# Kernel tuning notes

Measured on AMD Instinct MI355X. Metric: run time of the kernel, lower is better.

Reference implementation:

```python
import jax, jax.numpy as jnp
import numpy as np

DIM = 1024
NUM_HEADS = 16
WINDOW_SIZE = 512
HEAD_DIM = DIM // NUM_HEADS
SCALE = HEAD_DIM ** (-0.5)


def setup_inputs() -> dict:
    key = jax.random.key(0)
    kq, kk, kv = jax.random.split(key, 3)
    shape = (2, NUM_HEADS, 2048, HEAD_DIM)
    q = jax.random.normal(kq, shape, dtype=jnp.float32)
    k = jax.random.normal(kk, shape, dtype=jnp.float32)
    v = jax.random.normal(kv, shape, dtype=jnp.float32)
    return {"q": q, "k": k, "v": v}


def reference(q, k, v):
    B, H, N, D = q.shape
    pos = jnp.arange(N)
    # causal + sliding window: col <= row and col >= row - w + 1
    window_mask = (pos[None, :] <= pos[:, None]) & (pos[None, :] >= pos[:, None] - WINDOW_SIZE + 1)  # (N, N)
    attn = jnp.einsum("bhnd,bhmd->bhnm", q, k) * SCALE  # (B, H, N, N)
    attn = jnp.where(window_mask[None, None], attn, -jnp.inf)
    attn = jax.nn.softmax(attn, axis=-1)
    attn = jnp.nan_to_num(attn, nan=0.0)
    return jnp.einsum("bhnm,bhmd->bhnd", attn, v)
```

## Files before the change

kernel.cpp:

```cpp
#include <hip/hip_runtime.h>
#include <math.h>


#define SEQ 2048
#define HD  64
#define LDR 72

typedef short short8 __attribute__((ext_vector_type(8)));
typedef float f32x4  __attribute__((ext_vector_type(4)));
typedef int   i32x4  __attribute__((ext_vector_type(4)));

static __device__ inline unsigned short f2bf(float f){
  union{float f; unsigned u;} un; un.f=f;
  return (unsigned short)((un.u + 0x7FFFu + ((un.u>>16)&1u))>>16);
}
static __device__ inline int swz(int row){ return (row&3)|(((row>>3)&1)<<2); }

static __device__ __forceinline__ void gll16(const unsigned short* g, unsigned short* l){
  __builtin_amdgcn_global_load_lds(
    (const __attribute__((address_space(1))) unsigned int*)(const void*)g,
    (__attribute__((address_space(3))) unsigned int*)(void*)l, 16, 0, 0);
}

__global__ __launch_bounds__(256) void swa_prep(
    const float* __restrict__ k, const float* __restrict__ v,
    unsigned short* __restrict__ Kb, unsigned short* __restrict__ Vtb)
{
  const int tid=threadIdx.x, bid=blockIdx.x;
  const float C=0.18033688011112042f;

  if(bid<1024){
    const long tbase=(long)bid*4096;
    #pragma unroll
    for(int i=0;i<2;++i){
      int id=i*256+tid, r=id>>3, lc=id&7;
      float4 f0=*(const float4*)(k+tbase+r*64+lc*8);
      float4 f1=*(const float4*)(k+tbase+r*64+lc*8+4);
      unsigned short hh[8];
      hh[0]=f2bf(f0.x*C); hh[1]=f2bf(f0.y*C); hh[2]=f2bf(f0.z*C); hh[3]=f2bf(f0.w*C);
      hh[4]=f2bf(f1.x*C); hh[5]=f2bf(f1.y*C); hh[6]=f2bf(f1.z*C); hh[7]=f2bf(f1.w*C);
      *(uint4*)(Kb+tbase+r*64+(long)((lc^swz(r))*8))=*(uint4*)hh;
    }
  } else {
    __shared__ unsigned short Vs[64*68];
    const long tbase=(long)(bid-1024)*4096;
    #pragma unroll
    for(int i=0;i<2;++i){
      int id=i*256+tid, r=id>>3, c=id&7;
      int phys=(c^(r>>3))&7;
      float4 f0=*(const float4*)(v+tbase+r*64+c*8);
      float4 f1=*(const float4*)(v+tbase+r*64+c*8+4);
      ushort4 a,b;
      a.x=f2bf(f0.x); a.y=f2bf(f0.y); a.z=f2bf(f0.z); a.w=f2bf(f0.w);
      b.x=f2bf(f1.x); b.y=f2bf(f1.y); b.z=f2bf(f1.z); b.w=f2bf(f1.w);
      *(ushort4*)&Vs[r*68+phys*8]  =a;
      *(ushort4*)&Vs[r*68+phys*8+4]=b;
    }
    __syncthreads();
    #pragma unroll
    for(int i=0;i<2;++i){
      int id=i*256+tid, d=id>>3, lc=id&7;
      unsigned short t8[8];
      #pragma unroll
      for(int e=0;e<8;++e){
        int key=lc*8+e;
        int phys=((d>>3)^lc)&7;
        t8[e]=Vs[key*68 + phys*8 + (d&7)];
      }
      *(uint4*)(Vtb+tbase+d*64+(long)((lc^swz(d))*8))=*(uint4*)t8;
    }
  }
}

__global__ __launch_bounds__(512) void swa_main(
    const float* __restrict__ q,
    const unsigned short* __restrict__ Kb,
    const unsigned short* __restrict__ Vtb,
    float* __restrict__ out)
{
  __shared__ unsigned short Ks[2][8192];
  __shared__ unsigned short Vsh[2][8192];

  const int tid=threadIdx.x, bid=blockIdx.x;
  const int mt=bid&7, bh=bid>>3, m0=mt*256;
  const long base=(long)bh*SEQ*HD;
  const int wv=tid>>6, lane=tid&63, quad=lane>>4, l16=lane&15;
  const int qr0=m0+wv*32+l16;

  short8 qa[2][2];
  #pragma unroll
  for(int s=0;s<2;++s){
    const float* qp=q+base+(long)(qr0+s*16)*HD+quad*8;
    #pragma unroll
    for(int kk=0;kk<2;++kk){
      float4 f0=*(const float4*)(qp+kk*32);
      float4 f1=*(const float4*)(qp+kk*32+4);
      short8 a;
      a[0]=(short)f2bf(f0.x); a[1]=(short)f2bf(f0.y);
      a[2]=(short)f2bf(f0.z); a[3]=(short)f2bf(f0.w);
      a[4]=(short)f2bf(f1.x); a[5]=(short)f2bf(f1.y);
      a[6]=(short)f2bf(f1.z); a[7]=(short)f2bf(f1.w);
      qa[s][kk]=a;
    }
  }

  const int rbase=8*(l16>>2)+(l16&3);
  const int swk=(l16&3)|(((l16>>2)&1)<<2);
  const int swv=(l16&3)|(((l16>>3)&1)<<2);
  int kaoff[2][4], vboff[2][4];
  #pragma unroll
  for(int kk=0;kk<2;++kk){
    #pragma unroll
    for(int nt=0;nt<4;++nt)
      kaoff[kk][nt]=(rbase+(nt&1)*4+(nt>>1)*32)*64+(((quad+4*kk)^swk)*8);
    #pragma unroll
    for(int dt=0;dt<4;++dt)
      vboff[kk][dt]=(dt*16+l16)*64+(((quad+4*kk)^swv)*8);
  }

  const unsigned short* Kt=Kb +(long)bh*32*4096;
  const unsigned short* Vt=Vtb+(long)bh*32*4096;
  const int seg=tid*8;

  f32x4 oacc[2][4];
  #pragma unroll
  for(int s=0;s<2;++s)
    #pragma unroll
    for(int dt=0;dt<4;++dt) oacc[s][dt]=(f32x4){0.f,0.f,0.f,0.f};
  float lrun[2]={0.f,0.f};

  const int Tb =4*mt+3;
  const int Tlo=(4*mt>8)?(4*mt-8):0;
  const int npairs=(Tb-Tlo+1)>>1;
  const int myTb =4*mt+(wv>>1);
  const bool clip=(myTb>=8);
  const int myTlo=clip?(myTb-8):0;

  {
    const long o=(long)Tlo*4096;
    gll16(Kt+o+seg,      &Ks[0][seg]);
    gll16(Kt+o+4096+seg, &Ks[0][4096+seg]);
    gll16(Vt+o+seg,      &Vsh[0][seg]);
    gll16(Vt+o+4096+seg, &Vsh[0][4096+seg]);
  }
  __syncthreads();

  for(int p=0;p<npairs;++p){
    const int buf=p&1;
    if(p+1<npairs){
      const long o=(long)(Tlo+2*(p+1))*4096;
      gll16(Kt+o+seg,      &Ks[buf^1][seg]);
      gll16(Kt+o+4096+seg, &Ks[buf^1][4096+seg]);
      gll16(Vt+o+seg,      &Vsh[buf^1][seg]);
      gll16(Vt+o+4096+seg, &Vsh[buf^1][4096+seg]);
    }
    #pragma unroll
    for(int sub=0;sub<2;++sub){
      const int t=Tlo+2*p+sub;
      if(t>=myTlo && t<=myTb){
        const int tb_off=sub*4096;
        short8 ka[2][4], vb[4][2];
        #pragma unroll
        for(int kk=0;kk<2;++kk)
          #pragma unroll
          for(int nt=0;nt<4;++nt)
            ka[kk][nt]=*(const short8*)&Ks[buf][tb_off+kaoff[kk][nt]];
        #pragma unroll
        for(int dt=0;dt<4;++dt)
          #pragma unroll
          for(int kk=0;kk<2;++kk)
            vb[dt][kk]=*(const short8*)&Vsh[buf][tb_off+vboff[kk][dt]];

        const bool msk=(t==myTb)||(clip&&t==myTlo);
        #pragma unroll
        for(int s=0;s<2;++s){
          const int qrow=qr0+s*16;
          f32x4 sacc[4];
          #pragma unroll
          for(int nt=0;nt<4;++nt) sacc[nt]=(f32x4){0.f,0.f,0.f,0.f};
          #pragma unroll
          for(int kk=0;kk<2;++kk)
            #pragma unroll
            for(int nt=0;nt<4;++nt)
              sacc[nt]=__builtin_amdgcn_mfma_f32_16x16x32_bf16(ka[kk][nt],qa[s][kk],sacc[nt],0,0,0);

          unsigned pp[8];
          float ls=0.f;
          #pragma unroll
          for(int nt=0;nt<4;++nt){
            float e0,e1,e2,e3;
            e0=__builtin_amdgcn_exp2f(sacc[nt][0]);
            e1=__builtin_amdgcn_exp2f(sacc[nt][1]);
            e2=__builtin_amdgcn_exp2f(sacc[nt][2]);
            e3=__builtin_amdgcn_exp2f(sacc[nt][3]);
            if(msk){
              const int kb0=t*64+8*quad+(nt&1)*4+(nt>>1)*32;
              #pragma unroll
              for(int r=0;r<4;++r){
                const int key=kb0+r;
                const bool valid=(key<=qrow)&&(key+511>=qrow);
                float* ep=(r==0)?&e0:(r==1)?&e1:(r==2)?&e2:&e3;
                *ep = valid ? *ep : 0.f;
              }
            }
            ls+=e0+e1+e2+e3;
            pp[nt*2+0]=(__float_as_uint(e1)&0xFFFF0000u)|(__float_as_uint(e0)>>16);
            pp[nt*2+1]=(__float_as_uint(e3)&0xFFFF0000u)|(__float_as_uint(e2)>>16);
          }
          lrun[s]+=ls;
          i32x4 i0={(int)pp[0],(int)pp[1],(int)pp[2],(int)pp[3]};
          i32x4 i1={(int)pp[4],(int)pp[5],(int)pp[6],(int)pp[7]};
          short8 pa0=*(short8*)&i0;
          short8 pa1=*(short8*)&i1;
          #pragma unroll
          for(int dt=0;dt<4;++dt){
            oacc[s][dt]=__builtin_amdgcn_mfma_f32_16x16x32_bf16(pa0,vb[dt][0],oacc[s][dt],0,0,0);
            oacc[s][dt]=__builtin_amdgcn_mfma_f32_16x16x32_bf16(pa1,vb[dt][1],oacc[s][dt],0,0,0);
          }
        }
      }
    }
    __syncthreads();
  }

  #pragma unroll
  for(int s=0;s<2;++s){
    float l=lrun[s];
    l+=__shfl_xor(l,16);
    l+=__shfl_xor(l,32);
    float linv=1.0f/l;
    #pragma unroll
    for(int r=0;r<4;++r){
      float lr=__shfl(linv,quad*4+r);
      const int orow=m0+wv*32+s*16+quad*4+r;
      #pragma unroll
      for(int dt=0;dt<4;++dt)
        out[base+(long)orow*HD+dt*16+l16]=oacc[s][dt][r]*lr;
    }
  }
}

__global__ __launch_bounds__(256) void swa_fwd(
    const float* __restrict__ q, const float* __restrict__ k,
    const float* __restrict__ v, float* __restrict__ out)
{
  __shared__ short Qs[64*LDR];
  __shared__ short Ps[64*LDR];
  __shared__ short Ksh[2][64*LDR];
  __shared__ short Vtr[2][HD*LDR];

  const int tid=threadIdx.x, bid=blockIdx.x;
  const int mtile=bid&31, bh=bid>>5, m0=mtile*64;
  const long base=(long)bh*SEQ*HD;
  const int wv=tid>>6, lane=tid&63, quad=lane>>4, l16=lane&15;
  const int dcol=lane;

  {
    const float4* qg=(const float4*)(q+base+(long)m0*HD);
    #pragma unroll
    for(int i=0;i<4;++i){
      int idx=i*256+tid, r=idx>>4, c4=idx&15;
      float4 f=qg[idx];
      ushort4 hh; hh.x=f2bf(f.x); hh.y=f2bf(f.y); hh.z=f2bf(f.z); hh.w=f2bf(f.w);
      *(ushort4*)&Qs[r*LDR+c4*4]=hh;
    }
  }
  const int tb=mtile, tlo=(tb>8)?(tb-8):0;
  float4 kreg[4]; float vcol[4][4];
  {
    const float4* kg=(const float4*)(k+base+(long)(tlo*64)*HD);
    const float*  vg=v+base+(long)(tlo*64)*HD;
    #pragma unroll
    for(int i=0;i<4;++i) kreg[i]=kg[i*256+tid];
    #pragma unroll
    for(int g=0;g<4;++g){ int r0=wv*4+g*16;
      #pragma unroll
      for(int j=0;j<4;++j) vcol[g][j]=vg[(r0+j)*HD+dcol]; }
  }
  __syncthreads();
  short8 qa[2];
  #pragma unroll
  for(int kk=0;kk<2;++kk)
    qa[kk]=*(const short8*)&Qs[(wv*16+l16)*LDR+kk*32+quad*8];
  {
    #pragma unroll
    for(int i=0;i<4;++i){
      int idx=i*256+tid, r=idx>>4, c4=idx&15;
      float4 fk=kreg[i];
      ushort4 hk; hk.x=f2bf(fk.x); hk.y=f2bf(fk.y); hk.z=f2bf(fk.z); hk.w=f2bf(fk.w);
      *(ushort4*)&Ksh[0][r*LDR+c4*4]=hk;
    }
    #pragma unroll
    for(int g=0;g<4;++g){ int r0=wv*4+g*16;
      ushort4 hv; hv.x=f2bf(vcol[g][0]); hv.y=f2bf(vcol[g][1]);
                  hv.z=f2bf(vcol[g][2]); hv.w=f2bf(vcol[g][3]);
      *(ushort4*)&Vtr[0][dcol*LDR+r0]=hv; }
  }
  float lrun[4]={0.f,0.f,0.f,0.f};
  f32x4 oacc[4];
  #pragma unroll
  for(int dt=0;dt<4;++dt) oacc[dt]=(f32x4){0.f,0.f,0.f,0.f};
  __syncthreads();

  for(int t=tlo;t<=tb;++t){
    const int buf=(t-tlo)&1, j0=t*64;
    f32x4 sacc[4];
    #pragma unroll
    for(int nt=0;nt<4;++nt) sacc[nt]=(f32x4){0.f,0.f,0.f,0.f};
    #pragma unroll
    for(int kk=0;kk<2;++kk){
      #pragma unroll
      for(int nt=0;nt<4;++nt){
        short8 kb=*(const short8*)&Ksh[buf][(nt*16+l16)*LDR+kk*32+quad*8];
        sacc[nt]=__builtin_amdgcn_mfma_f32_16x16x32_bf16(qa[kk],kb,sacc[nt],0,0,0);
      }
    }
    if(t<tb){
      const float4* kg=(const float4*)(k+base+(long)((t+1)*64)*HD);
      const float*  vg=v+base+(long)((t+1)*64)*HD;
      #pragma unroll
      for(int i=0;i<4;++i) kreg[i]=kg[i*256+tid];
      #pragma unroll
      for(int g=0;g<4;++g){ int r0=wv*4+g*16;
        #pragma unroll
        for(int j=0;j<4;++j) vcol[g][j]=vg[(r0+j)*HD+dcol]; }
    }
    #pragma unroll
    for(int r=0;r<4;++r){
      const int grr=m0+wv*16+quad*4+r;
      #pragma unroll
      for(int nt=0;nt<4;++nt){
        const int gc=j0+nt*16+l16;
        float e=exp2f(sacc[nt][r]*0.18033688011112042f);
        float p=((gc<=grr)&&(gc>=grr-511))?e:0.f;
        lrun[r]+=p;
        Ps[(wv*16+quad*4+r)*LDR+nt*16+l16]=(short)f2bf(p);
      }
    }
    __syncthreads();
    #pragma unroll
    for(int kk=0;kk<2;++kk){
      short8 pa=*(const short8*)&Ps[(wv*16+l16)*LDR+kk*32+quad*8];
      #pragma unroll
      for(int dt=0;dt<4;++dt){
        short8 vb=*(const short8*)&Vtr[buf][(dt*16+l16)*LDR+kk*32+quad*8];
        oacc[dt]=__builtin_amdgcn_mfma_f32_16x16x32_bf16(pa,vb,oacc[dt],0,0,0);
      }
    }
    if(t<tb){
      #pragma unroll
      for(int i=0;i<4;++i){
        int idx=i*256+tid, r=idx>>4, c4=idx&15;
        float4 fk=kreg[i];
        ushort4 hk; hk.x=f2bf(fk.x); hk.y=f2bf(fk.y); hk.z=f2bf(fk.z); hk.w=f2bf(fk.w);
        *(ushort4*)&Ksh[buf^1][r*LDR+c4*4]=hk;
      }
      #pragma unroll
      for(int g=0;g<4;++g){ int r0=wv*4+g*16;
        ushort4 hv; hv.x=f2bf(vcol[g][0]); hv.y=f2bf(vcol[g][1]);
                    hv.z=f2bf(vcol[g][2]); hv.w=f2bf(vcol[g][3]);
        *(ushort4*)&Vtr[buf^1][dcol*LDR+r0]=hv; }
    }
    __syncthreads();
  }
  #pragma unroll
  for(int r=0;r<4;++r){
    float s=lrun[r];
    s+=__shfl_xor(s,1); s+=__shfl_xor(s,2); s+=__shfl_xor(s,4); s+=__shfl_xor(s,8);
    lrun[r]=(s>0.f)?(1.f/s):0.f;
  }
  #pragma unroll
  for(int r=0;r<4;++r){
    const int row=m0+wv*16+quad*4+r;
    #pragma unroll
    for(int dt=0;dt<4;++dt)
      out[base+(long)row*HD+dt*16+l16]=oacc[dt][r]*lrun[r];
  }
}

extern "C" void kernel_launch(void* const* d_in, const int* in_sizes, int n_in,
                              void* d_out, int out_size, void* d_ws, size_t ws_size,
                              hipStream_t stream) {
  (void)in_sizes; (void)n_in; (void)out_size;
  const float* q=(const float*)d_in[0];
  const float* k=(const float*)d_in[1];
  const float* v=(const float*)d_in[2];
  float* o=(float*)d_out;
  const size_t NEED = 2ull*32*2048*64*2;
  if (ws_size>=NEED){
    unsigned short* Kb =(unsigned short*)d_ws;
    unsigned short* Vtb=Kb+32ull*2048*64;
    hipLaunchKernelGGL(swa_prep, dim3(2048), dim3(256), 0, stream, k, v, Kb, Vtb);
    hipLaunchKernelGGL(swa_main, dim3(256),  dim3(512), 0, stream, q, Kb, Vtb, o);
  } else {
    hipLaunchKernelGGL(swa_fwd, dim3(1024), dim3(256), 0, stream, q, k, v, o);
  }
}
```

Measured before the change: 114.3 us.

## Halve query tile to 128 rows and stream one key tile per step

```diff
diff --git a/kernel.cpp b/kernel.cpp
--- a/kernel.cpp
+++ b/kernel.cpp
@@ -72,17 +72,17 @@
   }
 }
 
-__global__ __launch_bounds__(512) void swa_main(
+__global__ __launch_bounds__(256) void swa_main(
     const float* __restrict__ q,
     const unsigned short* __restrict__ Kb,
     const unsigned short* __restrict__ Vtb,
     float* __restrict__ out)
 {
-  __shared__ unsigned short Ks[2][8192];
-  __shared__ unsigned short Vsh[2][8192];
+  __shared__ unsigned short Ks[2][4096];
+  __shared__ unsigned short Vsh[2][4096];
 
   const int tid=threadIdx.x, bid=blockIdx.x;
-  const int mt=bid&7, bh=bid>>3, m0=mt*256;
+  const int mt=bid&15, bh=bid>>4, m0=mt*128;
   const long base=(long)bh*SEQ*HD;
   const int wv=tid>>6, lane=tid&63, quad=lane>>4, l16=lane&15;
   const int qr0=m0+wv*32+l16;
@@ -129,94 +129,84 @@
     for(int dt=0;dt<4;++dt) oacc[s][dt]=(f32x4){0.f,0.f,0.f,0.f};
   float lrun[2]={0.f,0.f};
 
-  const int Tb =4*mt+3;
-  const int Tlo=(4*mt>8)?(4*mt-8):0;
-  const int npairs=(Tb-Tlo+1)>>1;
-  const int myTb =4*mt+(wv>>1);
+  const int Tb =2*mt+1;
+  const int Tlo=(2*mt>8)?(2*mt-8):0;
+  const int myTb=2*mt+(wv>>1);
   const bool clip=(myTb>=8);
   const int myTlo=clip?(myTb-8):0;
 
   {
     const long o=(long)Tlo*4096;
     gll16(Kt+o+seg,      &Ks[0][seg]);
-    gll16(Kt+o+4096+seg, &Ks[0][4096+seg]);
+    gll16(Kt+o+2048+seg, &Ks[0][2048+seg]);
     gll16(Vt+o+seg,      &Vsh[0][seg]);
-    gll16(Vt+o+4096+seg, &Vsh[0][4096+seg]);
+    gll16(Vt+o+2048+seg, &Vsh[0][2048+seg]);
   }
   __syncthreads();
 
-  for(int p=0;p<npairs;++p){
-    const int buf=p&1;
-    if(p+1<npairs){
-      const long o=(long)(Tlo+2*(p+1))*4096;
+  for(int t=Tlo;t<=Tb;++t){
+    const int buf=(t-Tlo)&1;
+    if(t<Tb){
+      const long o=(long)(t+1)*4096;
       gll16(Kt+o+seg,      &Ks[buf^1][seg]);
-      gll16(Kt+o+4096+seg, &Ks[buf^1][4096+seg]);
+      gll16(Kt+o+2048+seg, &Ks[buf^1][2048+seg]);
       gll16(Vt+o+seg,      &Vsh[buf^1][seg]);
-      gll16(Vt+o+4096+seg, &Vsh[buf^1][4096+seg]);
-    }
-    #pragma unroll
-    for(int sub=0;sub<2;++sub){
-      const int t=Tlo+2*p+sub;
-      if(t>=myTlo && t<=myTb){
-        const int tb_off=sub*4096;
-        short8 ka[2][4], vb[4][2];
+      gll16(Vt+o+2048+seg, &Vsh[buf^1][2048+seg]);
+    }
+    if(t>=myTlo && t<=myTb){
+      short8 ka[2][4], vb[4][2];
+      #pragma unroll
+      for(int kk=0;kk<2;++kk)
+        #pragma unroll
+        for(int nt=0;nt<4;++nt)
+          ka[kk][nt]=*(const short8*)&Ks[buf][kaoff[kk][nt]];
+      #pragma unroll
+      for(int dt=0;dt<4;++dt)
+        #pragma unroll
+        for(int kk=0;kk<2;++kk)
+          vb[dt][kk]=*(const short8*)&Vsh[buf][vboff[kk][dt]];
+
+      const bool msk=(t==myTb)||(clip&&t==myTlo);
+      #pragma unroll
+      for(int s=0;s<2;++s){
+        const int qrow=qr0+s*16;
+        f32x4 sacc[4];
+        #pragma unroll
+        for(int nt=0;nt<4;++nt) sacc[nt]=(f32x4){0.f,0.f,0.f,0.f};
         #pragma unroll
         for(int kk=0;kk<2;++kk)
           #pragma unroll
           for(int nt=0;nt<4;++nt)
-            ka[kk][nt]=*(const short8*)&Ks[buf][tb_off+kaoff[kk][nt]];
-        #pragma unroll
-        for(int dt=0;dt<4;++dt)
-          #pragma unroll
-          for(int kk=0;kk<2;++kk)
-            vb[dt][kk]=*(const short8*)&Vsh[buf][tb_off+vboff[kk][dt]];
-
-        const bool msk=(t==myTb)||(clip&&t==myTlo);
-        #pragma unroll
-        for(int s=0;s<2;++s){
-          const int qrow=qr0+s*16;
-          f32x4 sacc[4];
-          #pragma unroll
-          for(int nt=0;nt<4;++nt) sacc[nt]=(f32x4){0.f,0.f,0.f,0.f};
-          #pragma unroll
-          for(int kk=0;kk<2;++kk)
-            #pragma unroll
-            for(int nt=0;nt<4;++nt)
-              sacc[nt]=__builtin_amdgcn_mfma_f32_16x16x32_bf16(ka[kk][nt],qa[s][kk],sacc[nt],0,0,0);
-
-          unsigned pp[8];
-          float ls=0.f;
-          #pragma unroll
-          for(int nt=0;nt<4;++nt){
-            float e0,e1,e2,e3;
-            e0=__builtin_amdgcn_exp2f(sacc[nt][0]);
-            e1=__builtin_amdgcn_exp2f(sacc[nt][1]);
-            e2=__builtin_amdgcn_exp2f(sacc[nt][2]);
-            e3=__builtin_amdgcn_exp2f(sacc[nt][3]);
-            if(msk){
-              const int kb0=t*64+8*quad+(nt&1)*4+(nt>>1)*32;
-              #pragma unroll
-              for(int r=0;r<4;++r){
-                const int key=kb0+r;
-                const bool valid=(key<=qrow)&&(key+511>=qrow);
-                float* ep=(r==0)?&e0:(r==1)?&e1:(r==2)?&e2:&e3;
-                *ep = valid ? *ep : 0.f;
-              }
-            }
-            ls+=e0+e1+e2+e3;
-            pp[nt*2+0]=(__float_as_uint(e1)&0xFFFF0000u)|(__float_as_uint(e0)>>16);
-            pp[nt*2+1]=(__float_as_uint(e3)&0xFFFF0000u)|(__float_as_uint(e2)>>16);
+            sacc[nt]=__builtin_amdgcn_mfma_f32_16x16x32_bf16(ka[kk][nt],qa[s][kk],sacc[nt],0,0,0);
+
+        unsigned pp[8];
+        float ls=0.f;
+        #pragma unroll
+        for(int nt=0;nt<4;++nt){
+          float e0=__builtin_amdgcn_exp2f(sacc[nt][0]);
+          float e1=__builtin_amdgcn_exp2f(sacc[nt][1]);
+          float e2=__builtin_amdgcn_exp2f(sacc[nt][2]);
+          float e3=__builtin_amdgcn_exp2f(sacc[nt][3]);
+          if(msk){
+            const int kb0=t*64+8*quad+(nt&1)*4+(nt>>1)*32;
+            e0=((kb0+0<=qrow)&&(kb0+0+511>=qrow))?e0:0.f;
+            e1=((kb0+1<=qrow)&&(kb0+1+511>=qrow))?e1:0.f;
+            e2=((kb0+2<=qrow)&&(kb0+2+511>=qrow))?e2:0.f;
+            e3=((kb0+3<=qrow)&&(kb0+3+511>=qrow))?e3:0.f;
           }
-          lrun[s]+=ls;
-          i32x4 i0={(int)pp[0],(int)pp[1],(int)pp[2],(int)pp[3]};
-          i32x4 i1={(int)pp[4],(int)pp[5],(int)pp[6],(int)pp[7]};
-          short8 pa0=*(short8*)&i0;
-          short8 pa1=*(short8*)&i1;
-          #pragma unroll
-          for(int dt=0;dt<4;++dt){
-            oacc[s][dt]=__builtin_amdgcn_mfma_f32_16x16x32_bf16(pa0,vb[dt][0],oacc[s][dt],0,0,0);
-            oacc[s][dt]=__builtin_amdgcn_mfma_f32_16x16x32_bf16(pa1,vb[dt][1],oacc[s][dt],0,0,0);
-          }
+          ls+=e0+e1+e2+e3;
+          pp[nt*2+0]=(__float_as_uint(e1)&0xFFFF0000u)|(__float_as_uint(e0)>>16);
+          pp[nt*2+1]=(__float_as_uint(e3)&0xFFFF0000u)|(__float_as_uint(e2)>>16);
+        }
+        lrun[s]+=ls;
+        i32x4 i0={(int)pp[0],(int)pp[1],(int)pp[2],(int)pp[3]};
+        i32x4 i1={(int)pp[4],(int)pp[5],(int)pp[6],(int)pp[7]};
+        short8 pa0=*(short8*)&i0;
+        short8 pa1=*(short8*)&i1;
+        #pragma unroll
+        for(int dt=0;dt<4;++dt){
+          oacc[s][dt]=__builtin_amdgcn_mfma_f32_16x16x32_bf16(pa0,vb[dt][0],oacc[s][dt],0,0,0);
+          oacc[s][dt]=__builtin_amdgcn_mfma_f32_16x16x32_bf16(pa1,vb[dt][1],oacc[s][dt],0,0,0);
         }
       }
     }
@@ -391,7 +381,7 @@
     unsigned short* Kb =(unsigned short*)d_ws;
     unsigned short* Vtb=Kb+32ull*2048*64;
     hipLaunchKernelGGL(swa_prep, dim3(2048), dim3(256), 0, stream, k, v, Kb, Vtb);
-    hipLaunchKernelGGL(swa_main, dim3(256),  dim3(512), 0, stream, q, Kb, Vtb, o);
+    hipLaunchKernelGGL(swa_main, dim3(512),  dim3(256), 0, stream, q, Kb, Vtb, o);
   } else {
     hipLaunchKernelGGL(swa_fwd, dim3(1024), dim3(256), 0, stream, q, k, v, o);
   }
```

Result: no change. 116.5 us (+1.9%).
